# Performance work log

Measured on AMD Instinct MI355X. Metric: run time of the kernel, lower is better.

## Reference

```python
import jax, jax.numpy as jnp
import numpy as np

NUM_GROUPS = 32
EPS = 1e-5

def group_norm(x, weight, bias):
    # x: [B, C, H, W]
    b, c, h, w = x.shape
    g = NUM_GROUPS
    xg = x.reshape(b, g, (c // g) * h * w)
    mean = xg.mean(axis=-1, keepdims=True)
    var = xg.var(axis=-1, keepdims=True)
    xn = ((xg - mean) * jax.lax.rsqrt(var + EPS)).reshape(b, c, h, w)
    return xn * weight[None, :, None, None] + bias[None, :, None, None]

def setup_inputs() -> dict:
    key = jax.random.key(0)
    ks = jax.random.split(key, 4)
    B, C, H, W = 4, 256, 64, 64
    x = jax.random.normal(ks[0], (B, C, H, W), dtype=jnp.float32)
    gn_weight = jnp.ones((C,), dtype=jnp.float32)
    gn_bias = jnp.zeros((C,), dtype=jnp.float32)
    # 1x1 conv == linear over channel dim; init ~ kaiming-uniform-ish scale
    qkv_weight = jax.random.normal(ks[1], (3 * C, C), dtype=jnp.float32) / np.sqrt(C)
    qkv_bias = jnp.zeros((3 * C,), dtype=jnp.float32)
    out_weight = jax.random.normal(ks[2], (C, C), dtype=jnp.float32) / np.sqrt(C)
    out_bias = jnp.zeros((C,), dtype=jnp.float32)
    return {"x": x, "gn_weight": gn_weight, "gn_bias": gn_bias,
            "qkv_weight": qkv_weight, "qkv_bias": qkv_bias,
            "out_weight": out_weight, "out_bias": out_bias}

def reference(x, gn_weight, gn_bias, qkv_weight, qkv_bias, out_weight, out_bias):
    b, c, h, w = x.shape
    n = h * w
    xn = group_norm(x, gn_weight, gn_bias)
    # 1x1 conv QKV projection: [B, 3C, H, W]
    qkv = jnp.einsum('bchw,oc->bohw', xn, qkv_weight) + qkv_bias[None, :, None, None]
    q, k, v = jnp.split(qkv, 3, axis=1)
    q = q.transpose(0, 2, 3, 1).reshape(b, n, c)   # [B, N, C]
    k = k.reshape(b, c, n)                         # [B, C, N]
    v = v.transpose(0, 2, 3, 1).reshape(b, n, c)   # [B, N, C]
    scores = jnp.einsum('bnc,bcm->bnm', q, k) * (c ** -0.5)  # [B, N, N]
    attn = jax.nn.softmax(scores, axis=-1)
    out = jnp.einsum('bnm,bmc->bnc', attn, v)      # [B, N, C]
    out = out.reshape(b, h, w, c).transpose(0, 3, 1, 2)  # [B, C, H, W]
    out = jnp.einsum('bchw,oc->bohw', out, out_weight) + out_bias[None, :, None, None]
    return out + x
```

## Files before the change

### kernel.cpp

```cpp
#include <hip/hip_runtime.h>
#include <math.h>

#define B_   4
#define C_   256
#define G_   32
#define CPG  8
#define N_   4096
#define NPG  (CPG * N_)
#define EPS  1e-5f
#define SCALE 0.0625f

typedef __attribute__((ext_vector_type(8)))  __bf16 bf16x8;
typedef __attribute__((ext_vector_type(4)))  __bf16 bf16x4;
typedef __attribute__((ext_vector_type(16))) float  f32x16;

__global__ __launch_bounds__(256) void gn_stats_kernel(const float* __restrict__ x,
                                                       float* __restrict__ part) {
    int bid = blockIdx.x;
    int bg = bid >> 2, seg = bid & 3;
    const float4* xp4 = (const float4*)(x + (size_t)bg * NPG) + seg * 2048;
    int tid = threadIdx.x;

    float s = 0.f, ss = 0.f;
    for (int i = tid; i < 2048; i += 256) {
        float4 t = xp4[i];
        s  += t.x + t.y + t.z + t.w;
        ss += t.x * t.x + t.y * t.y + t.z * t.z + t.w * t.w;
    }
    #pragma unroll
    for (int off = 32; off; off >>= 1) {
        s  += __shfl_xor(s, off, 64);
        ss += __shfl_xor(ss, off, 64);
    }
    __shared__ float rs[2][4];
    int wave = tid >> 6, lane = tid & 63;
    if (lane == 0) { rs[0][wave] = s; rs[1][wave] = ss; }
    __syncthreads();
    if (tid == 0) {
        part[bid * 2]     = rs[0][0] + rs[0][1] + rs[0][2] + rs[0][3];
        part[bid * 2 + 1] = rs[1][0] + rs[1][1] + rs[1][2] + rs[1][3];
    }
}

__global__ __launch_bounds__(256) void gn_apply_kernel(const float* __restrict__ x,
                                                       const float* __restrict__ w,
                                                       const float* __restrict__ bia,
                                                       const float* __restrict__ part,
                                                       __bf16* __restrict__ xnb) {
    int bid = blockIdx.x;
    int bg = bid >> 4, seg = bid & 15;
    int b = bg >> 5, g = bg & 31;
    float s  = part[(bg * 4 + 0) * 2] + part[(bg * 4 + 1) * 2]
             + part[(bg * 4 + 2) * 2] + part[(bg * 4 + 3) * 2];
    float ss = part[(bg * 4 + 0) * 2 + 1] + part[(bg * 4 + 1) * 2 + 1]
             + part[(bg * 4 + 2) * 2 + 1] + part[(bg * 4 + 3) * 2 + 1];
    float mean = s / (float)NPG;
    float var  = ss / (float)NPG - mean * mean;
    float rstd = rsqrtf(var + EPS);

    const float* xp = x + (size_t)bg * NPG;
    int n = seg * 256 + threadIdx.x;

    bf16x8 pk;
    #pragma unroll
    for (int cc = 0; cc < 8; cc++) {
        float sc = rstd * w[g * CPG + cc];
        float sh = bia[g * CPG + cc] - mean * sc;
        pk[cc] = (__bf16)(xp[(size_t)cc * N_ + n] * sc + sh);
    }
    size_t idx = ((((size_t)(b * 128 + (n >> 5)) * 16 + (g >> 1)) * 2 + (g & 1))
                  * 32 + (n & 31)) * 8;
    *(bf16x8*)(xnb + idx) = pk;
}

__global__ __launch_bounds__(256) void qkv_kernel(const __bf16* __restrict__ xnb,
                                                  const float* __restrict__ W,
                                                  const float* __restrict__ bias,
                                                  __bf16* __restrict__ q,
                                                  __bf16* __restrict__ k,
                                                  __bf16* __restrict__ v) {
    int b = blockIdx.z, ot = blockIdx.y, nc = blockIdx.x;
    int tid = threadIdx.x, wv = tid >> 6, lane = tid & 63;
    int n31 = lane & 31, q2 = lane >> 5;
    int B0 = ot * 128 + wv * 32;

    bf16x8 wf[16];
    const float* wp = W + (size_t)(B0 + n31) * C_;
    #pragma unroll
    for (int ks = 0; ks < 16; ks++) {
        float4 t0 = *(const float4*)(wp + ks * 16 + q2 * 8);
        float4 t1 = *(const float4*)(wp + ks * 16 + q2 * 8 + 4);
        bf16x8 f;
        f[0] = (__bf16)t0.x; f[1] = (__bf16)t0.y; f[2] = (__bf16)t0.z; f[3] = (__bf16)t0.w;
        f[4] = (__bf16)t1.x; f[5] = (__bf16)t1.y; f[6] = (__bf16)t1.z; f[7] = (__bf16)t1.w;
        wf[ks] = f;
    }

    float bv[16], bvv = 0.f;
    if (ot < 4) {
        #pragma unroll
        for (int gI = 0; gI < 4; gI++)
            #pragma unroll
            for (int j = 0; j < 4; j++)
                bv[gI * 4 + j] = bias[B0 + gI * 8 + 4 * q2 + j];
    } else {
        bvv = bias[B0 + n31];
    }

    const __bf16* xb = xnb + (size_t)b * 128 * 8192;

    for (int t = 0; t < 4; t++) {
        int nt = nc * 4 + t;
        const __bf16* xg = xb + (size_t)nt * 8192 + q2 * 256 + n31 * 8;
        bf16x8 xf[16];
        #pragma unroll
        for (int ks = 0; ks < 16; ks++) xf[ks] = *(const bf16x8*)(xg + ks * 512);

        f32x16 acc;
        #pragma unroll
        for (int i = 0; i < 16; i++) acc[i] = 0.f;
        if (ot < 4) {
            #pragma unroll
            for (int ks = 0; ks < 16; ks++)
                acc = __builtin_amdgcn_mfma_f32_32x32x16_bf16(wf[ks], xf[ks], acc, 0, 0, 0);
        } else {
            #pragma unroll
            for (int ks = 0; ks < 16; ks++)
                acc = __builtin_amdgcn_mfma_f32_32x32x16_bf16(xf[ks], wf[ks], acc, 0, 0, 0);
        }

        if (ot < 4) {
            int ocb = (ot < 2) ? B0 : (B0 - 256);
            __bf16* dst = (ot < 2) ? q : k;
            bool isq = (ot < 2);
            #pragma unroll
            for (int gI = 0; gI < 4; gI++) {
                bf16x4 pk;
                #pragma unroll
                for (int j = 0; j < 4; j++) {
                    float y = acc[gI * 4 + j] + bv[gI * 4 + j];
                    if (isq) y *= SCALE;
                    pk[j] = (__bf16)y;
                }
                size_t idx = ((((size_t)(b * 128 + nt) * 16 + ((ocb >> 4) + (gI >> 1))) * 2
                               + (gI & 1)) * 32 + n31) * 8 + 4 * q2;
                *(bf16x4*)(dst + idx) = pk;
            }
        } else {
            int ocb = B0 - 512;
            #pragma unroll
            for (int gI = 0; gI < 4; gI++) {
                bf16x4 pk;
                #pragma unroll
                for (int j = 0; j < 4; j++)
                    pk[j] = (__bf16)(acc[gI * 4 + j] + bvv);
                size_t idx = (((((size_t)(b * 128 + nt) * 2 + (gI >> 1)) * 2 + (gI & 1)) * 8
                               + (ocb >> 5)) * 32 + n31) * 8 + 4 * q2;
                *(bf16x4*)(v + idx) = pk;
            }
        }
    }
}

#define PSTR 68

__global__ __launch_bounds__(512, 4) void attn_kernel(const __bf16* __restrict__ q,
                                                      const __bf16* __restrict__ k,
                                                      const __bf16* __restrict__ v,
                                                      float* __restrict__ ao0,
                                                      float* __restrict__ ao1,
                                                      float* __restrict__ l0,
                                                      float* __restrict__ l1) {
    __shared__ __bf16 p_lds[2][64 * PSTR];
    __shared__ float  l_lds[64];

    int bid   = blockIdx.x;
    int xcd   = bid & 7;
    int b     = xcd >> 1;
    int split = xcd & 1;
    int qt    = bid >> 3;
    int n0    = qt * 64;

    int tid = threadIdx.x;
    int wid = tid >> 6, lane = tid & 63;
    int n31 = lane & 31, q2 = lane >> 5;

    if (tid < 64) l_lds[tid] = 0.f;

    const size_t BSTR = (size_t)N_ * C_;

    if (wid < 4) {
        int kt = wid & 1;
        int rt = wid >> 1;
        const __bf16* qg = q + (size_t)(b * 128 + qt * 2 + rt) * 8192
                           + q2 * 256 + n31 * 8;
        bf16x8 qf[16];
        #pragma unroll
        for (int ks = 0; ks < 16; ks++) qf[ks] = *(const bf16x8*)(qg + ks * 512);

        const __bf16* kbase = k + (size_t)(b * 128 + split * 64 + kt) * 8192
                              + q2 * 256 + n31 * 8;
        float l_acc = 0.f;

        for (int ch = 0; ch < 32; ch++) {
            __syncthreads();
            const __bf16* kg = kbase + (size_t)ch * 16384;
            f32x16 s;
            #pragma unroll
            for (int i = 0; i < 16; i++) s[i] = 0.f;
            #pragma unroll
            for (int ks = 0; ks < 16; ks++) {
                bf16x8 kf = *(const bf16x8*)(kg + ks * 512);
                s = __builtin_amdgcn_mfma_f32_32x32x16_bf16(kf, qf[ks], s, 0, 0, 0);
            }
            __bf16* pbuf = p_lds[ch & 1];
            #pragma unroll
            for (int g = 0; g < 4; g++) {
                bf16x4 pw;
                #pragma unroll
                for (int j = 0; j < 4; j++) {
                    float p = __expf(s[g * 4 + j]);
                    l_acc += p;
                    pw[j] = (__bf16)p;
                }
                *(bf16x4*)(pbuf + (rt * 32 + n31) * PSTR + kt * 32 + 8 * g + 4 * q2) = pw;
            }
        }
        atomicAdd(&l_lds[rt * 32 + n31], l_acc);
        __syncthreads();
        if (tid < 64) {
            float* lp = split ? l1 : l0;
            lp[(size_t)b * N_ + n0 + tid] = l_lds[tid];
        }
    } else {
        int cw = wid - 4;
        const __bf16* vbase = v + (size_t)b * BSTR + (size_t)split * 524288
                              + (size_t)q2 * 2048 + n31 * 8;
        f32x16 o_acc[2][2];
        #pragma unroll
        for (int ct = 0; ct < 2; ct++)
            #pragma unroll
            for (int rt = 0; rt < 2; rt++)
                #pragma unroll
                for (int i = 0; i < 16; i++) o_acc[ct][rt][i] = 0.f;

        for (int ch = 0; ch < 32; ch++) {
            __syncthreads();
            if (ch > 0) {
                int cc = ch - 1;
                const __bf16* pbuf = p_lds[cc & 1];
                #pragma unroll
                for (int ct = 0; ct < 2; ct++) {
                    bf16x8 vf[4];
                    #pragma unroll
                    for (int ks4 = 0; ks4 < 4; ks4++) {
                        size_t off = (size_t)(cc * 2 + (ks4 >> 1)) * 8192
                                   + (size_t)(ks4 & 1) * 4096 + (cw * 2 + ct) * 256;
                        vf[ks4] = *(const bf16x8*)(vbase + off);
                    }
                    #pragma unroll
                    for (int rt = 0; rt < 2; rt++) {
                        const __bf16* pb = pbuf + (rt * 32 + n31) * PSTR + q2 * 8;
                        #pragma unroll
                        for (int ks4 = 0; ks4 < 4; ks4++) {
                            bf16x8 pf = *(const bf16x8*)(pb + ks4 * 16);
                            o_acc[ct][rt] = __builtin_amdgcn_mfma_f32_32x32x16_bf16(
                                vf[ks4], pf, o_acc[ct][rt], 0, 0, 0);
                        }
                    }
                }
            }
        }
        __syncthreads();
        {
            int cc = 31;
            const __bf16* pbuf = p_lds[1];
            #pragma unroll
            for (int ct = 0; ct < 2; ct++) {
                bf16x8 vf[4];
                #pragma unroll
                for (int ks4 = 0; ks4 < 4; ks4++) {
                    size_t off = (size_t)(cc * 2 + (ks4 >> 1)) * 8192
                               + (size_t)(ks4 & 1) * 4096 + (cw * 2 + ct) * 256;
                    vf[ks4] = *(const bf16x8*)(vbase + off);
                }
                #pragma unroll
                for (int rt = 0; rt < 2; rt++) {
                    const __bf16* pb = pbuf + (rt * 32 + n31) * PSTR + q2 * 8;
                    #pragma unroll
                    for (int ks4 = 0; ks4 < 4; ks4++) {
                        bf16x8 pf = *(const bf16x8*)(pb + ks4 * 16);
                        o_acc[ct][rt] = __builtin_amdgcn_mfma_f32_32x32x16_bf16(
                            vf[ks4], pf, o_acc[ct][rt], 0, 0, 0);
                    }
                }
            }
        }
        float* aop = split ? ao1 : ao0;
        #pragma unroll
        for (int ct = 0; ct < 2; ct++)
            #pragma unroll
            for (int rt = 0; rt < 2; rt++)
                #pragma unroll
                for (int g = 0; g < 4; g++) {
                    float4 st;
                    st.x = o_acc[ct][rt][g * 4 + 0];
                    st.y = o_acc[ct][rt][g * 4 + 1];
                    st.z = o_acc[ct][rt][g * 4 + 2];
                    st.w = o_acc[ct][rt][g * 4 + 3];
                    size_t idx = ((((((size_t)(b * 64 + qt) * 4 + cw) * 2 + ct) * 2 + rt)
                                   * 4 + g) * 2 + q2) * 128 + n31 * 4;
                    *(float4*)(aop + idx) = st;
                }
    }
}

__global__ __launch_bounds__(256) void proj_kernel(const float* __restrict__ ao0,
                                                   const float* __restrict__ ao1,
                                                   const float* __restrict__ l0p,
                                                   const float* __restrict__ l1p,
                                                   const float* __restrict__ W2,
                                                   const float* __restrict__ bias,
                                                   const float* __restrict__ x,
                                                   float* __restrict__ out) {
    int b = blockIdx.z, ot = blockIdx.y, nc = blockIdx.x;
    int tid = threadIdx.x, wv = tid >> 6, lane = tid & 63;
    int n31 = lane & 31, q2 = lane >> 5;
    int B0 = ot * 128 + wv * 32;

    bf16x8 wf[16];
    const float* wp = W2 + (size_t)(B0 + n31) * C_;
    #pragma unroll
    for (int ks = 0; ks < 16; ks++) {
        float4 t0 = *(const float4*)(wp + ks * 16 + q2 * 8);
        float4 t1 = *(const float4*)(wp + ks * 16 + q2 * 8 + 4);
        bf16x8 f;
        f[0] = (__bf16)t0.x; f[1] = (__bf16)t0.y; f[2] = (__bf16)t0.z; f[3] = (__bf16)t0.w;
        f[4] = (__bf16)t1.x; f[5] = (__bf16)t1.y; f[6] = (__bf16)t1.z; f[7] = (__bf16)t1.w;
        wf[ks] = f;
    }
    float bv[16];
    #pragma unroll
    for (int r = 0; r < 16; r++) bv[r] = bias[B0 + (r & 3) + 8 * (r >> 2) + 4 * q2];

    for (int t = 0; t < 4; t++) {
        int nt = nc * 4 + t;
        int qt = nt >> 1, rtile = nt & 1;
        int n = nt * 32 + n31;
        float inv = 1.0f / (l0p[(size_t)b * N_ + n] + l1p[(size_t)b * N_ + n]);

        bf16x8 xf[16];
        #pragma unroll
        for (int ks = 0; ks < 16; ks++) {
            int oct = ks * 2 + q2;
            int cw = oct >> 3, ct = (oct >> 2) & 1, ga = oct & 3;
            size_t base = ((((((size_t)(b * 64 + qt) * 4 + cw) * 2 + ct) * 2 + rtile)
                            * 4 + ga) * 2) * 128 + n31 * 4;
            float4 a0 = *(const float4*)(ao0 + base);
            float4 b0 = *(const float4*)(ao0 + base + 128);
            float4 a1 = *(const float4*)(ao1 + base);
            float4 b1 = *(const float4*)(ao1 + base + 128);
            bf16x8 f;
            f[0] = (__bf16)((a0.x + a1.x) * inv);
            f[1] = (__bf16)((a0.y + a1.y) * inv);
            f[2] = (__bf16)((a0.z + a1.z) * inv);
            f[3] = (__bf16)((a0.w + a1.w) * inv);
            f[4] = (__bf16)((b0.x + b1.x) * inv);
            f[5] = (__bf16)((b0.y + b1.y) * inv);
            f[6] = (__bf16)((b0.z + b1.z) * inv);
            f[7] = (__bf16)((b0.w + b1.w) * inv);
            xf[ks] = f;
        }

        f32x16 acc;
        #pragma unroll
        for (int i = 0; i < 16; i++) acc[i] = 0.f;
        #pragma unroll
        for (int ks = 0; ks < 16; ks++)
            acc = __builtin_amdgcn_mfma_f32_32x32x16_bf16(wf[ks], xf[ks], acc, 0, 0, 0);

        #pragma unroll
        for (int r = 0; r < 16; r++) {
            int o = B0 + (r & 3) + 8 * (r >> 2) + 4 * q2;
            size_t idx = ((size_t)(b * C_ + o)) * N_ + nt * 32 + n31;
            out[idx] = acc[r] + bv[r] + x[idx];
        }
    }
}

extern "C" void kernel_launch(void* const* d_in, const int* in_sizes, int n_in,
                              void* d_out, int out_size, void* d_ws, size_t ws_size,
                              hipStream_t stream) {
    const float* x     = (const float*)d_in[0];
    const float* gn_w  = (const float*)d_in[1];
    const float* gn_b  = (const float*)d_in[2];
    const float* qkv_w = (const float*)d_in[3];
    const float* qkv_b = (const float*)d_in[4];
    const float* out_w = (const float*)d_in[5];
    const float* out_b = (const float*)d_in[6];
    float* out = (float*)d_out;

    const size_t SZ = (size_t)B_ * C_ * N_;
    char* base = (char*)d_ws;
    float*  ao0 = (float*)base;
    float*  ao1 = (float*)(base + SZ * 4);
    __bf16* xnb = (__bf16*)base;
    __bf16* qb  = (__bf16*)(base + 2 * SZ * 4);
    __bf16* kb  = qb + SZ;
    __bf16* vb  = kb + SZ;
    float*  l0  = (float*)(base + 2 * SZ * 4 + 3 * SZ * 2);
    float*  l1  = l0 + B_ * N_;
    float*  part = l1 + B_ * N_;

    gn_stats_kernel<<<dim3(512), 256, 0, stream>>>(x, part);
    gn_apply_kernel<<<dim3(2048), 256, 0, stream>>>(x, gn_w, gn_b, part, xnb);
    qkv_kernel<<<dim3(32, 6, B_), 256, 0, stream>>>(xnb, qkv_w, qkv_b, qb, kb, vb);
    attn_kernel<<<dim3(512), 512, 0, stream>>>(qb, kb, vb, ao0, ao1, l0, l1);
    proj_kernel<<<dim3(32, 2, B_), 256, 0, stream>>>(ao0, ao1, l0, l1, out_w, out_b, x, out);
}
```

Before: 226.9 us.

## Stage Q in LDS and double key-chunk width per attention pipeline step

```diff
diff --git a/kernel.cpp b/kernel.cpp
--- a/kernel.cpp
+++ b/kernel.cpp
@@ -162,7 +162,7 @@
     }
 }
 
-#define PSTR 68
+#define PSTR2 132
 
 __global__ __launch_bounds__(512, 4) void attn_kernel(const __bf16* __restrict__ q,
                                                       const __bf16* __restrict__ k,
@@ -171,8 +171,9 @@
                                                       float* __restrict__ ao1,
                                                       float* __restrict__ l0,
                                                       float* __restrict__ l1) {
-    __shared__ __bf16 p_lds[2][64 * PSTR];
-    __shared__ float  l_lds[64];
+    __shared__ __align__(16) __bf16 q_lds[2 * 8192];
+    __shared__ __align__(16) __bf16 p_lds[2][64 * PSTR2];
+    __shared__ float l_lds[64];
 
     int bid   = blockIdx.x;
     int xcd   = bid & 7;
@@ -185,48 +186,58 @@
     int wid = tid >> 6, lane = tid & 63;
     int n31 = lane & 31, q2 = lane >> 5;
 
+    {
+        const __bf16* qsrc = q + (size_t)(b * 128 + qt * 2) * 8192;
+        #pragma unroll
+        for (int r = 0; r < 4; r++) {
+            int e = (r * 512 + tid) * 8;
+            *(bf16x8*)(q_lds + e) = *(const bf16x8*)(qsrc + e);
+        }
+    }
     if (tid < 64) l_lds[tid] = 0.f;
 
     const size_t BSTR = (size_t)N_ * C_;
 
     if (wid < 4) {
-        int kt = wid & 1;
-        int rt = wid >> 1;
-        const __bf16* qg = q + (size_t)(b * 128 + qt * 2 + rt) * 8192
-                           + q2 * 256 + n31 * 8;
-        bf16x8 qf[16];
-        #pragma unroll
-        for (int ks = 0; ks < 16; ks++) qf[ks] = *(const bf16x8*)(qg + ks * 512);
-
-        const __bf16* kbase = k + (size_t)(b * 128 + split * 64 + kt) * 8192
-                              + q2 * 256 + n31 * 8;
-        float l_acc = 0.f;
-
-        for (int ch = 0; ch < 32; ch++) {
+        int kt = wid;
+        const __bf16* ql0 = q_lds + q2 * 256 + n31 * 8;
+        const __bf16* kb0 = k + (size_t)(b * 128 + split * 64 + kt) * 8192
+                            + q2 * 256 + n31 * 8;
+        float l_acc0 = 0.f, l_acc1 = 0.f;
+
+        for (int ch = 0; ch < 16; ch++) {
             __syncthreads();
-            const __bf16* kg = kbase + (size_t)ch * 16384;
-            f32x16 s;
-            #pragma unroll
-            for (int i = 0; i < 16; i++) s[i] = 0.f;
+            const __bf16* kg = kb0 + (size_t)ch * 32768;
+            f32x16 s0, s1;
+            #pragma unroll
+            for (int i = 0; i < 16; i++) { s0[i] = 0.f; s1[i] = 0.f; }
             #pragma unroll
             for (int ks = 0; ks < 16; ks++) {
-                bf16x8 kf = *(const bf16x8*)(kg + ks * 512);
-                s = __builtin_amdgcn_mfma_f32_32x32x16_bf16(kf, qf[ks], s, 0, 0, 0);
-            }
-            __bf16* pbuf = p_lds[ch & 1];
+                bf16x8 kf  = *(const bf16x8*)(kg + ks * 512);
+                bf16x8 qa0 = *(const bf16x8*)(ql0 + ks * 512);
+                bf16x8 qa1 = *(const bf16x8*)(ql0 + 8192 + ks * 512);
+                s0 = __builtin_amdgcn_mfma_f32_32x32x16_bf16(kf, qa0, s0, 0, 0, 0);
+                s1 = __builtin_amdgcn_mfma_f32_32x32x16_bf16(kf, qa1, s1, 0, 0, 0);
+            }
+            __bf16* pbuf  = p_lds[ch & 1];
+            __bf16* prow0 = pbuf + n31 * PSTR2 + kt * 32 + 4 * q2;
+            __bf16* prow1 = pbuf + (32 + n31) * PSTR2 + kt * 32 + 4 * q2;
             #pragma unroll
             for (int g = 0; g < 4; g++) {
-                bf16x4 pw;
+                bf16x4 pw0, pw1;
                 #pragma unroll
                 for (int j = 0; j < 4; j++) {
-                    float p = __expf(s[g * 4 + j]);
-                    l_acc += p;
-                    pw[j] = (__bf16)p;
-                }
-                *(bf16x4*)(pbuf + (rt * 32 + n31) * PSTR + kt * 32 + 8 * g + 4 * q2) = pw;
-            }
-        }
-        atomicAdd(&l_lds[rt * 32 + n31], l_acc);
+                    float p0 = __expf(s0[g * 4 + j]);
+                    float p1 = __expf(s1[g * 4 + j]);
+                    l_acc0 += p0; l_acc1 += p1;
+                    pw0[j] = (__bf16)p0; pw1[j] = (__bf16)p1;
+                }
+                *(bf16x4*)(prow0 + 8 * g) = pw0;
+                *(bf16x4*)(prow1 + 8 * g) = pw1;
+            }
+        }
+        atomicAdd(&l_lds[n31], l_acc0);
+        atomicAdd(&l_lds[32 + n31], l_acc1);
         __syncthreads();
         if (tid < 64) {
             float* lp = split ? l1 : l0;
@@ -244,55 +255,85 @@
                 #pragma unroll
                 for (int i = 0; i < 16; i++) o_acc[ct][rt][i] = 0.f;
 
-        for (int ch = 0; ch < 32; ch++) {
+        for (int ch = 0; ch < 16; ch++) {
+            bf16x8 vf0[8];
+            if (ch > 0) {
+                int cc = ch - 1;
+                #pragma unroll
+                for (int ks4 = 0; ks4 < 8; ks4++) {
+                    size_t off = (size_t)(cc * 4 + (ks4 >> 1)) * 8192
+                               + (size_t)(ks4 & 1) * 4096 + (cw * 2 + 0) * 256;
+                    vf0[ks4] = *(const bf16x8*)(vbase + off);
+                }
+            }
             __syncthreads();
             if (ch > 0) {
                 int cc = ch - 1;
                 const __bf16* pbuf = p_lds[cc & 1];
                 #pragma unroll
-                for (int ct = 0; ct < 2; ct++) {
-                    bf16x8 vf[4];
+                for (int rt = 0; rt < 2; rt++) {
+                    const __bf16* pb = pbuf + (rt * 32 + n31) * PSTR2 + q2 * 8;
                     #pragma unroll
-                    for (int ks4 = 0; ks4 < 4; ks4++) {
-                        size_t off = (size_t)(cc * 2 + (ks4 >> 1)) * 8192
-                                   + (size_t)(ks4 & 1) * 4096 + (cw * 2 + ct) * 256;
-                        vf[ks4] = *(const bf16x8*)(vbase + off);
+                    for (int ks4 = 0; ks4 < 8; ks4++) {
+                        bf16x8 pf = *(const bf16x8*)(pb + ks4 * 16);
+                        o_acc[0][rt] = __builtin_amdgcn_mfma_f32_32x32x16_bf16(
+                            vf0[ks4], pf, o_acc[0][rt], 0, 0, 0);
                     }
+                }
+                bf16x8 vf1[8];
+                #pragma unroll
+                for (int ks4 = 0; ks4 < 8; ks4++) {
+                    size_t off = (size_t)(cc * 4 + (ks4 >> 1)) * 8192
+                               + (size_t)(ks4 & 1) * 4096 + (cw * 2 + 1) * 256;
+                    vf1[ks4] = *(const bf16x8*)(vbase + off);
+                }
+                #pragma unroll
+                for (int rt = 0; rt < 2; rt++) {
+                    const __bf16* pb = pbuf + (rt * 32 + n31) * PSTR2 + q2 * 8;
                     #pragma unroll
-                    for (int rt = 0; rt < 2; rt++) {
-                        const __bf16* pb = pbuf + (rt * 32 + n31) * PSTR + q2 * 8;
-                        #pragma unroll
-                        for (int ks4 = 0; ks4 < 4; ks4++) {
-                            bf16x8 pf = *(const bf16x8*)(pb + ks4 * 16);
-                            o_acc[ct][rt] = __builtin_amdgcn_mfma_f32_32x32x16_bf16(
-                                vf[ks4], pf, o_acc[ct][rt], 0, 0, 0);
-                        }
+                    for (int ks4 = 0; ks4 < 8; ks4++) {
+                        bf16x8 pf = *(const bf16x8*)(pb + ks4 * 16);
+                        o_acc[1][rt] = __builtin_amdgcn_mfma_f32_32x32x16_bf16(
+                            vf1[ks4], pf, o_acc[1][rt], 0, 0, 0);
                     }
                 }
             }
+        }
+        bf16x8 vt0[8];
+        #pragma unroll
+        for (int ks4 = 0; ks4 < 8; ks4++) {
+            size_t off = (size_t)(15 * 4 + (ks4 >> 1)) * 8192
+                       + (size_t)(ks4 & 1) * 4096 + (cw * 2 + 0) * 256;
+            vt0[ks4] = *(const bf16x8*)(vbase + off);
         }
         __syncthreads();
         {
-            int cc = 31;
             const __bf16* pbuf = p_lds[1];
             #pragma unroll
-            for (int ct = 0; ct < 2; ct++) {
-                bf16x8 vf[4];
-                #pragma unroll
-                for (int ks4 = 0; ks4 < 4; ks4++) {
-                    size_t off = (size_t)(cc * 2 + (ks4 >> 1)) * 8192
-                               + (size_t)(ks4 & 1) * 4096 + (cw * 2 + ct) * 256;
-                    vf[ks4] = *(const bf16x8*)(vbase + off);
-                }
-                #pragma unroll
-                for (int rt = 0; rt < 2; rt++) {
-                    const __bf16* pb = pbuf + (rt * 32 + n31) * PSTR + q2 * 8;
-                    #pragma unroll
-                    for (int ks4 = 0; ks4 < 4; ks4++) {
-                        bf16x8 pf = *(const bf16x8*)(pb + ks4 * 16);
-                        o_acc[ct][rt] = __builtin_amdgcn_mfma_f32_32x32x16_bf16(
-                            vf[ks4], pf, o_acc[ct][rt], 0, 0, 0);
-                    }
+            for (int rt = 0; rt < 2; rt++) {
+                const __bf16* pb = pbuf + (rt * 32 + n31) * PSTR2 + q2 * 8;
+                #pragma unroll
+                for (int ks4 = 0; ks4 < 8; ks4++) {
+                    bf16x8 pf = *(const bf16x8*)(pb + ks4 * 16);
+                    o_acc[0][rt] = __builtin_amdgcn_mfma_f32_32x32x16_bf16(
+                        vt0[ks4], pf, o_acc[0][rt], 0, 0, 0);
+                }
+            }
+            bf16x8 vt1[8];
+            #pragma unroll
+            for (int ks4 = 0; ks4 < 8; ks4++) {
+                size_t off = (size_t)(15 * 4 + (ks4 >> 1)) * 8192
+                           + (size_t)(ks4 & 1) * 4096 + (cw * 2 + 1) * 256;
+                vt1[ks4] = *(const bf16x8*)(vbase + off);
+            }
+            #pragma unroll
+            for (int rt = 0; rt < 2; rt++) {
+                const __bf16* pb = pbuf + (rt * 32 + n31) * PSTR2 + q2 * 8;
+                #pragma unroll
+                for (int ks4 = 0; ks4 < 8; ks4++) {
+                    bf16x8 pf = *(const bf16x8*)(pb + ks4 * 16);
+                    o_acc[1][rt] = __builtin_amdgcn_mfma_f32_32x32x16_bf16(
+                        vt1[ks4], pf, o_acc[1][rt], 0, 0, 0);
                 }
             }
         }
```

Result: no change. 225.8 us (-0.5%).

## Stage K tiles into LDS with async global_load_lds double buffering in attention

Applied to the files above, without the earlier changes.

```diff
diff --git a/kernel.cpp b/kernel.cpp
--- a/kernel.cpp
+++ b/kernel.cpp
@@ -9,6 +9,7 @@
 #define NPG  (CPG * N_)
 #define EPS  1e-5f
 #define SCALE 0.0625f
+#define NCH  32
 
 typedef __attribute__((ext_vector_type(8)))  __bf16 bf16x8;
 typedef __attribute__((ext_vector_type(4)))  __bf16 bf16x4;
@@ -162,17 +163,20 @@
     }
 }
 
-#define PSTR 68
+__device__ __forceinline__ void stage16(const __bf16* g, __bf16* l) {
+    __builtin_amdgcn_global_load_lds(
+        (const __attribute__((address_space(1))) unsigned int*)g,
+        (__attribute__((address_space(3))) unsigned int*)l, 16, 0, 0);
+}
 
 __global__ __launch_bounds__(512, 4) void attn_kernel(const __bf16* __restrict__ q,
                                                       const __bf16* __restrict__ k,
                                                       const __bf16* __restrict__ v,
                                                       float* __restrict__ ao0,
                                                       float* __restrict__ ao1,
-                                                      float* __restrict__ l0,
-                                                      float* __restrict__ l1) {
-    __shared__ __bf16 p_lds[2][64 * PSTR];
-    __shared__ float  l_lds[64];
+                                                      float* __restrict__ lpart) {
+    __shared__ __align__(16) __bf16 k_lds[2][16384];
+    __shared__ __align__(16) __bf16 p_lds[2][64 * 64];
 
     int bid   = blockIdx.x;
     int xcd   = bid & 7;
@@ -185,9 +189,16 @@
     int wid = tid >> 6, lane = tid & 63;
     int n31 = lane & 31, q2 = lane >> 5;
 
-    if (tid < 64) l_lds[tid] = 0.f;
-
     const size_t BSTR = (size_t)N_ * C_;
+    const __bf16* kgbase = k + (size_t)(b * 128 + split * 64) * 8192
+                           + wid * 2048 + lane * 8;
+
+    {
+        __bf16* l = (__bf16*)k_lds[0] + wid * 2048;
+        #pragma unroll
+        for (int i = 0; i < 4; i++)
+            stage16(kgbase + i * 512, l + i * 512);
+    }
 
     if (wid < 4) {
         int kt = wid & 1;
@@ -198,40 +209,51 @@
         #pragma unroll
         for (int ks = 0; ks < 16; ks++) qf[ks] = *(const bf16x8*)(qg + ks * 512);
 
-        const __bf16* kbase = k + (size_t)(b * 128 + split * 64 + kt) * 8192
-                              + q2 * 256 + n31 * 8;
         float l_acc = 0.f;
-
-        for (int ch = 0; ch < 32; ch++) {
+        int prow = rt * 32 + n31;
+        int swz  = (prow & 7) << 4;
+        int klo  = kt * 8192 + q2 * 256 + n31 * 8;
+
+        for (int ch = 0; ch < NCH; ch++) {
             __syncthreads();
-            const __bf16* kg = kbase + (size_t)ch * 16384;
-            f32x16 s;
-            #pragma unroll
-            for (int i = 0; i < 16; i++) s[i] = 0.f;
-            #pragma unroll
-            for (int ks = 0; ks < 16; ks++) {
-                bf16x8 kf = *(const bf16x8*)(kg + ks * 512);
-                s = __builtin_amdgcn_mfma_f32_32x32x16_bf16(kf, qf[ks], s, 0, 0, 0);
-            }
-            __bf16* pbuf = p_lds[ch & 1];
-            #pragma unroll
-            for (int g = 0; g < 4; g++) {
+            if (ch < NCH - 1) {
+                const __bf16* g = kgbase + (size_t)(ch + 1) * 16384;
+                __bf16* l = (__bf16*)k_lds[(ch + 1) & 1] + wid * 2048;
+                #pragma unroll
+                for (int i = 0; i < 4; i++)
+                    stage16(g + i * 512, l + i * 512);
+            }
+            const __bf16* kl = (const __bf16*)k_lds[ch & 1] + klo;
+            f32x16 sa, sb;
+            #pragma unroll
+            for (int i = 0; i < 16; i++) { sa[i] = 0.f; sb[i] = 0.f; }
+            __builtin_amdgcn_s_setprio(1);
+            #pragma unroll
+            for (int i = 0; i < 8; i++) {
+                bf16x8 ka = *(const bf16x8*)(kl + i * 512);
+                bf16x8 kb = *(const bf16x8*)(kl + (i + 8) * 512);
+                sa = __builtin_amdgcn_mfma_f32_32x32x16_bf16(ka, qf[i], sa, 0, 0, 0);
+                sb = __builtin_amdgcn_mfma_f32_32x32x16_bf16(kb, qf[i + 8], sb, 0, 0, 0);
+            }
+            __builtin_amdgcn_s_setprio(0);
+            char* pbuf = (char*)p_lds[ch & 1];
+            #pragma unroll
+            for (int gI = 0; gI < 4; gI++) {
                 bf16x4 pw;
                 #pragma unroll
                 for (int j = 0; j < 4; j++) {
-                    float p = __expf(s[g * 4 + j]);
+                    float p = __expf(sa[gI * 4 + j] + sb[gI * 4 + j]);
                     l_acc += p;
                     pw[j] = (__bf16)p;
                 }
-                *(bf16x4*)(pbuf + (rt * 32 + n31) * PSTR + kt * 32 + 8 * g + 4 * q2) = pw;
-            }
-        }
-        atomicAdd(&l_lds[rt * 32 + n31], l_acc);
+                int off = prow * 128 + kt * 64 + 16 * gI + 8 * q2;
+                *(bf16x4*)(pbuf + (off ^ swz)) = pw;
+            }
+        }
         __syncthreads();
-        if (tid < 64) {
-            float* lp = split ? l1 : l0;
-            lp[(size_t)b * N_ + n0 + tid] = l_lds[tid];
-        }
+        l_acc += __shfl_down(l_acc, 32);
+        if (lane < 32)
+            lpart[((size_t)(split * 2 + kt) * B_ + b) * N_ + n0 + rt * 32 + lane] = l_acc;
     } else {
         int cw = wid - 4;
         const __bf16* vbase = v + (size_t)b * BSTR + (size_t)split * 524288
@@ -244,57 +266,75 @@
                 #pragma unroll
                 for (int i = 0; i < 16; i++) o_acc[ct][rt][i] = 0.f;
 
-        for (int ch = 0; ch < 32; ch++) {
-            __syncthreads();
+        for (int ch = 0; ch < NCH; ch++) {
+            bf16x8 vf[2][4];
             if (ch > 0) {
                 int cc = ch - 1;
-                const __bf16* pbuf = p_lds[cc & 1];
-                #pragma unroll
-                for (int ct = 0; ct < 2; ct++) {
-                    bf16x8 vf[4];
+                #pragma unroll
+                for (int ct = 0; ct < 2; ct++)
                     #pragma unroll
                     for (int ks4 = 0; ks4 < 4; ks4++) {
                         size_t off = (size_t)(cc * 2 + (ks4 >> 1)) * 8192
                                    + (size_t)(ks4 & 1) * 4096 + (cw * 2 + ct) * 256;
-                        vf[ks4] = *(const bf16x8*)(vbase + off);
+                        vf[ct][ks4] = *(const bf16x8*)(vbase + off);
                     }
+                asm volatile("" ::: "memory");
+            }
+            __syncthreads();
+            if (ch < NCH - 1) {
+                const __bf16* g = kgbase + (size_t)(ch + 1) * 16384;
+                __bf16* l = (__bf16*)k_lds[(ch + 1) & 1] + wid * 2048;
+                #pragma unroll
+                for (int i = 0; i < 4; i++)
+                    stage16(g + i * 512, l + i * 512);
+            }
+            if (ch > 0) {
+                const char* pbuf = (const char*)p_lds[(ch - 1) & 1];
+                __builtin_amdgcn_s_setprio(1);
+                #pragma unroll
+                for (int ct = 0; ct < 2; ct++)
                     #pragma unroll
                     for (int rt = 0; rt < 2; rt++) {
-                        const __bf16* pb = pbuf + (rt * 32 + n31) * PSTR + q2 * 8;
+                        int prow = rt * 32 + n31;
+                        int swz  = (prow & 7) << 4;
+                        int pbs  = prow * 128 + q2 * 16;
                         #pragma unroll
                         for (int ks4 = 0; ks4 < 4; ks4++) {
-                            bf16x8 pf = *(const bf16x8*)(pb + ks4 * 16);
+                            bf16x8 pf = *(const bf16x8*)(pbuf + ((pbs + ks4 * 32) ^ swz));
                             o_acc[ct][rt] = __builtin_amdgcn_mfma_f32_32x32x16_bf16(
-                                vf[ks4], pf, o_acc[ct][rt], 0, 0, 0);
+                                vf[ct][ks4], pf, o_acc[ct][rt], 0, 0, 0);
                         }
                     }
-                }
-            }
-        }
+                __builtin_amdgcn_s_setprio(0);
+            }
+        }
+        bf16x8 vt[2][4];
+        #pragma unroll
+        for (int ct = 0; ct < 2; ct++)
+            #pragma unroll
+            for (int ks4 = 0; ks4 < 4; ks4++) {
+                size_t off = (size_t)(31 * 2 + (ks4 >> 1)) * 8192
+                           + (size_t)(ks4 & 1) * 4096 + (cw * 2 + ct) * 256;
+                vt[ct][ks4] = *(const bf16x8*)(vbase + off);
+            }
+        asm volatile("" ::: "memory");
         __syncthreads();
         {
-            int cc = 31;
-            const __bf16* pbuf = p_lds[1];
-            #pragma unroll
-            for (int ct = 0; ct < 2; ct++) {
-                bf16x8 vf[4];
-                #pragma unroll
-                for (int ks4 = 0; ks4 < 4; ks4++) {
-                    size_t off = (size_t)(cc * 2 + (ks4 >> 1)) * 8192
-                               + (size_t)(ks4 & 1) * 4096 + (cw * 2 + ct) * 256;
-                    vf[ks4] = *(const bf16x8*)(vbase + off);
-                }
+            const char* pbuf = (const char*)p_lds[1];
+            #pragma unroll
+            for (int ct = 0; ct < 2; ct++)
                 #pragma unroll
                 for (int rt = 0; rt < 2; rt++) {
-                    const __bf16* pb = pbuf + (rt * 32 + n31) * PSTR + q2 * 8;
+                    int prow = rt * 32 + n31;
+                    int swz  = (prow & 7) << 4;
+                    int pbs  = prow * 128 + q2 * 16;
                     #pragma unroll
                     for (int ks4 = 0; ks4 < 4; ks4++) {
-                        bf16x8 pf = *(const bf16x8*)(pb + ks4 * 16);
+                        bf16x8 pf = *(const bf16x8*)(pbuf + ((pbs + ks4 * 32) ^ swz));
                         o_acc[ct][rt] = __builtin_amdgcn_mfma_f32_32x32x16_bf16(
-                            vf[ks4], pf, o_acc[ct][rt], 0, 0, 0);
+                            vt[ct][ks4], pf, o_acc[ct][rt], 0, 0, 0);
                     }
                 }
-            }
         }
         float* aop = split ? ao1 : ao0;
         #pragma unroll
@@ -317,8 +357,7 @@
 
 __global__ __launch_bounds__(256) void proj_kernel(const float* __restrict__ ao0,
                                                    const float* __restrict__ ao1,
-                                                   const float* __restrict__ l0p,
-                                                   const float* __restrict__ l1p,
+                                                   const float* __restrict__ lpart,
                                                    const float* __restrict__ W2,
                                                    const float* __restrict__ bias,
                                                    const float* __restrict__ x,
@@ -327,6 +366,7 @@
     int tid = threadIdx.x, wv = tid >> 6, lane = tid & 63;
     int n31 = lane & 31, q2 = lane >> 5;
     int B0 = ot * 128 + wv * 32;
+    const size_t BN = (size_t)B_ * N_;
 
     bf16x8 wf[16];
     const float* wp = W2 + (size_t)(B0 + n31) * C_;
@@ -347,7 +387,9 @@
         int nt = nc * 4 + t;
         int qt = nt >> 1, rtile = nt & 1;
         int n = nt * 32 + n31;
-        float inv = 1.0f / (l0p[(size_t)b * N_ + n] + l1p[(size_t)b * N_ + n]);
+        size_t ln = (size_t)b * N_ + n;
+        float lsum = lpart[ln] + lpart[BN + ln] + lpart[2 * BN + ln] + lpart[3 * BN + ln];
+        float inv = 1.0f / lsum;
 
         bf16x8 xf[16];
         #pragma unroll
@@ -408,13 +450,12 @@
     __bf16* qb  = (__bf16*)(base + 2 * SZ * 4);
     __bf16* kb  = qb + SZ;
     __bf16* vb  = kb + SZ;
-    float*  l0  = (float*)(base + 2 * SZ * 4 + 3 * SZ * 2);
-    float*  l1  = l0 + B_ * N_;
-    float*  part = l1 + B_ * N_;
+    float*  lpart = (float*)(base + 2 * SZ * 4 + 3 * SZ * 2);
+    float*  part  = lpart + 4 * (size_t)B_ * N_;
 
     gn_stats_kernel<<<dim3(512), 256, 0, stream>>>(x, part);
     gn_apply_kernel<<<dim3(2048), 256, 0, stream>>>(x, gn_w, gn_b, part, xnb);
     qkv_kernel<<<dim3(32, 6, B_), 256, 0, stream>>>(xnb, qkv_w, qkv_b, qb, kb, vb);
-    attn_kernel<<<dim3(512), 512, 0, stream>>>(qb, kb, vb, ao0, ao1, l0, l1);
-    proj_kernel<<<dim3(32, 2, B_), 256, 0, stream>>>(ao0, ao1, l0, l1, out_w, out_b, x, out);
-}
+    attn_kernel<<<dim3(512), 512, 0, stream>>>(qb, kb, vb, ao0, ao1, lpart);
+    proj_kernel<<<dim3(32, 2, B_), 256, 0, stream>>>(ao0, ao1, lpart, out_w, out_b, x, out);
+}
```

After: 227.9 us. No clear change (+0.5%).
